# Kernel optimization log

Measured on AMD Instinct MI355X. Metric: run time of the kernel, lower is better.

Reference implementation:

```python
import jax, jax.numpy as jnp
import numpy as np

KS = 3  # kernel_size
N, C_IN, C_OUT, H, W = 8, 64, 128, 256, 256


def _grid_sample_bilinear(img, gx, gy):
    """img [C,H,W]; gx, gy [Ho,Wo] normalized coords; align_corners=False, zero padding."""
    C, H_, W_ = img.shape
    ix = ((gx + 1.0) * W_ - 1.0) / 2.0
    iy = ((gy + 1.0) * H_ - 1.0) / 2.0
    x0 = jnp.floor(ix); y0 = jnp.floor(iy)
    x1 = x0 + 1.0;      y1 = y0 + 1.0
    wx1 = ix - x0; wx0 = 1.0 - wx1
    wy1 = iy - y0; wy0 = 1.0 - wy1

    def gather(yi, xi):
        valid = (xi >= 0) & (xi < W_) & (yi >= 0) & (yi < H_)
        xc = jnp.clip(xi, 0, W_ - 1).astype(jnp.int32)
        yc = jnp.clip(yi, 0, H_ - 1).astype(jnp.int32)
        v = img[:, yc, xc]  # [C,Ho,Wo]
        return v * valid[None].astype(img.dtype)

    out = (gather(y0, x0) * (wy0 * wx0)[None]
         + gather(y0, x1) * (wy0 * wx1)[None]
         + gather(y1, x0) * (wy1 * wx0)[None]
         + gather(y1, x1) * (wy1 * wx1)[None])
    return out


def setup_inputs() -> dict:
    key = jax.random.key(0)
    k1, k2, k3 = jax.random.split(key, 3)
    x = jax.random.normal(k1, (N, C_IN, H, W), dtype=jnp.float32)
    # offset conv: Conv2d(inc, 2*ks, ks, padding=(ks-1)//2, bias=False)
    offset_w = jax.random.normal(k2, (2 * KS, C_IN, KS, KS), dtype=jnp.float32) * 0.05
    # conv_kernel: Conv2d(inc, outc, kernel=(ks,1), stride=(ks,1), bias=False), kaiming fan_out
    fan_out = C_OUT * KS * 1
    conv_w = jax.random.normal(k3, (C_OUT, C_IN, KS, 1), dtype=jnp.float32) * np.sqrt(2.0 / fan_out)
    return {"x": x, "offset_w": offset_w, "conv_w": conv_w}


def reference(x, offset_w, conv_w):
    n, c, h, w = x.shape
    ks = KS
    pad = (ks - 1) // 2
    dn = ('NCHW', 'OIHW', 'NCHW')

    off = jax.lax.conv_general_dilated(x, offset_w, (1, 1), ((pad, pad), (pad, pad)),
                                       dimension_numbers=dn)  # [n,2ks,h,w]
    off = jnp.tanh(off).reshape(n, 2, ks, h, w)
    offset_y = off[:, 0]  # [n,ks,h,w]; x offsets are computed but unused in the original

    yc = (ks - 1) // 2
    # cumulative offsets radiating outward from the center row
    upper = jnp.cumsum(offset_y[:, yc:], axis=1)                       # indices yc..ks-1
    lower = jnp.cumsum(offset_y[:, :yc + 1][:, ::-1], axis=1)[:, ::-1]  # indices 0..yc
    y_new = jnp.concatenate([lower[:, :yc], upper], axis=1)            # [n,ks,h,w]

    # base grid replicates torch's repeat-then-reshape layout exactly:
    # flat pattern [-1,0,1,-1,0,1,...] of length ks*h*w, reshaped to (ks,h,w)
    vals = jnp.arange(-(ks - 1) // 2, (ks - 1) // 2 + 1, dtype=x.dtype)
    base = vals[jnp.arange(ks * h * w) % ks].reshape(ks, h, w)

    grid_y = (base[None] + y_new).reshape(n, ks * h, w)
    gy = grid_y / ((h - 1.0) / 2.0) - 1.0
    gx = jnp.full_like(gy, -1.0)  # grid_x is zeros -> 0/((w-1)/2) - 1 = -1

    sampled = jax.vmap(_grid_sample_bilinear)(x, gx, gy)  # [n,c,ks*h,w]

    out = jax.lax.conv_general_dilated(sampled, conv_w, (ks, 1), ((0, 0), (0, 0)),
                                       dimension_numbers=dn)  # [n,outc,h,w]
    return out
```

## Files before the change

### kernel.cpp

```cpp
#include <hip/hip_runtime.h>
#include <math.h>

#define H 256
#define W 256
#define NB 8
#define CIN 64
#define COUT 128
#define G 2
#define CPG 32

typedef float f4v __attribute__((ext_vector_type(4)));

__global__ __launch_bounds__(256) void koffset(const float* __restrict__ x,
                                               const float* __restrict__ offw,
                                               float* __restrict__ part) {
    __shared__ float tile[2][34 * 40];
    const int g = blockIdx.z & (G - 1);
    const int n = blockIdx.z / G;
    const int i0 = blockIdx.y * 32;
    const int j0 = blockIdx.x * 32;
    const int tid = threadIdx.x;
    const int li = tid >> 3;
    const int lj4 = (tid & 7) * 4;

    const int a1 = tid / 10, cv1 = tid - a1 * 10;
    const int p2 = tid + 256;
    const int a2 = p2 / 10, cv2 = p2 - a2 * 10;
    const bool have2 = (p2 < 340);

    const float* xbase = x + ((size_t)(n * CIN + g * CPG)) * (H * W);

    auto ld = [&](int a, int cv, const float* xp) -> float4 {
        int gi = i0 - 1 + a;
        int gj = j0 - 4 + cv * 4;
        if ((unsigned)gi < (unsigned)H && (unsigned)gj < (unsigned)W)
            return *(const float4*)(xp + gi * W + gj);
        return make_float4(0.f, 0.f, 0.f, 0.f);
    };

    float acc[3][4];
#pragma unroll
    for (int k = 0; k < 3; ++k)
#pragma unroll
        for (int d = 0; d < 4; ++d) acc[k][d] = 0.f;

    float4 r1 = ld(a1, cv1, xbase);
    float4 r2 = have2 ? ld(a2, cv2, xbase) : make_float4(0, 0, 0, 0);

    for (int c = 0; c < CPG; ++c) {
        float* buf = tile[c & 1];
        *(float4*)(buf + tid * 4) = r1;
        if (have2) *(float4*)(buf + p2 * 4) = r2;
        float4 r1n, r2n;
        if (c < CPG - 1) {
            const float* xpn = xbase + (size_t)(c + 1) * (H * W);
            r1n = ld(a1, cv1, xpn);
            r2n = have2 ? ld(a2, cv2, xpn) : make_float4(0, 0, 0, 0);
        }
        __syncthreads();
        const float* wp = offw + (g * CPG + c) * 9;
#pragma unroll
        for (int u = 0; u < 3; ++u) {
            float row[6];
#pragma unroll
            for (int m = 0; m < 6; ++m) row[m] = buf[(li + u) * 40 + 3 + lj4 + m];
#pragma unroll
            for (int k = 0; k < 3; ++k) {
                float w0 = wp[k * 576 + u * 3 + 0];
                float w1 = wp[k * 576 + u * 3 + 1];
                float w2 = wp[k * 576 + u * 3 + 2];
#pragma unroll
                for (int d = 0; d < 4; ++d)
                    acc[k][d] += row[d] * w0 + row[d + 1] * w1 + row[d + 2] * w2;
            }
        }
        r1 = r1n;
        r2 = r2n;
    }

    size_t base = (((size_t)g * NB + n) * 3) * (H * W) + (size_t)(i0 + li) * W + (j0 + lj4);
#pragma unroll
    for (int k = 0; k < 3; ++k) {
        float4 o = make_float4(acc[k][0], acc[k][1], acc[k][2], acc[k][3]);
        *(float4*)(part + base + (size_t)k * (H * W)) = o;
    }
}

__global__ __launch_bounds__(256) void kreduce(const float* __restrict__ part,
                                               float* __restrict__ ynew) {
    int idx = blockIdx.x * 256 + threadIdx.x;
    int n = idx >> 14;
    int hw4 = idx & 16383;
    size_t off = (size_t)hw4 * 4;
    float t[3][4];
#pragma unroll
    for (int k = 0; k < 3; ++k) {
        float4 s0 = *(const float4*)(part + (((size_t)0 * NB + n) * 3 + k) * (H * W) + off);
        float4 s1 = *(const float4*)(part + (((size_t)1 * NB + n) * 3 + k) * (H * W) + off);
        t[k][0] = tanhf(s0.x + s1.x);
        t[k][1] = tanhf(s0.y + s1.y);
        t[k][2] = tanhf(s0.z + s1.z);
        t[k][3] = tanhf(s0.w + s1.w);
    }
    size_t base = ((size_t)n * 3) * (H * W) + off;
    *(float4*)(ynew + base) =
        make_float4(t[0][0] + t[1][0], t[0][1] + t[1][1], t[0][2] + t[1][2], t[0][3] + t[1][3]);
    *(float4*)(ynew + base + (size_t)(H * W)) = make_float4(t[1][0], t[1][1], t[1][2], t[1][3]);
    *(float4*)(ynew + base + (size_t)2 * (H * W)) =
        make_float4(t[1][0] + t[2][0], t[1][1] + t[2][1], t[1][2] + t[2][2], t[1][3] + t[2][3]);
}

__global__ __launch_bounds__(256) void kpmat(const float* __restrict__ x,
                                             const float* __restrict__ convw,
                                             float* __restrict__ P) {
    __shared__ float xl[CIN * 4];
    __shared__ float wl[16 * 192];
    const int n = blockIdx.x >> 3;
    const int co0 = (blockIdx.x & 7) * 16;
    const int tid = threadIdx.x;
    {
        int ci = tid >> 2, y = tid & 3;
        xl[tid] = x[(((size_t)n * CIN + ci) * H + y) * W];
    }
    for (int p = tid; p < 16 * 192; p += 256) wl[p] = convw[co0 * 192 + p];
    __syncthreads();
    if (tid < 192) {
        int co = tid / 12, t = tid - co * 12;
        int r = t >> 2, y = t & 3;
        float s = 0.f;
#pragma unroll
        for (int ci = 0; ci < CIN; ++ci) s += wl[co * 192 + ci * 3 + r] * xl[ci * 4 + y];
        P[((size_t)n * COUT + co0 + co) * 16 + t] = s;
    }
}

__global__ __launch_bounds__(256) void kout(const float* __restrict__ ynew,
                                            const float* __restrict__ P,
                                            float* __restrict__ out) {
    __shared__ float Cs[12 * 256];
    __shared__ float Pl[128 * 16];
    const int n = blockIdx.y;
    const int i = blockIdx.x;
    const int tid = threadIdx.x;

    {
        const f4v* src = (const f4v*)(P + (size_t)n * COUT * 16);
        f4v* dst = (f4v*)Pl;
        dst[tid] = src[tid];
        dst[tid + 256] = src[tid + 256];
    }

    {
        const int j = tid;
        float c[12];
#pragma unroll
        for (int t = 0; t < 12; ++t) c[t] = 0.f;
#pragma unroll
        for (int r = 0; r < 3; ++r) {
            int rowi = 3 * i + r;
            int k = rowi >> 8;
            int i2 = rowi & 255;
            float g = (float)(((k + i2 + j) % 3) - 1) +
                      ynew[((size_t)n * 3 + k) * (H * W) + i2 * W + j];
            float gy = g / 127.5f - 1.0f;
            float iy = ((gy + 1.0f) * 256.0f - 1.0f) * 0.5f;
            float fy = floorf(iy);
            int y0 = (int)fy;
            float w1 = iy - fy;
            if ((unsigned)y0 < 4u) c[r * 4 + y0] += 0.5f * (1.0f - w1);
            int y1 = y0 + 1;
            if ((unsigned)y1 < 4u) c[r * 4 + y1] += 0.5f * w1;
        }
#pragma unroll
        for (int t = 0; t < 12; ++t) Cs[t * 256 + j] = c[t];
    }
    __syncthreads();

    const int jq = (tid & 63) * 4;
    const int cg = tid >> 6;
    float4 cc[12];
#pragma unroll
    for (int t = 0; t < 12; ++t) cc[t] = *(const float4*)&Cs[t * 256 + jq];

    float* op = out + (((size_t)n * COUT) * H + i) * W;
    for (int co = cg * 32; co < cg * 32 + 32; ++co) {
        const float4* pp = (const float4*)&Pl[co * 16];
        float4 P0 = pp[0], P1 = pp[1], P2 = pp[2];
        float pv[12] = {P0.x, P0.y, P0.z, P0.w, P1.x, P1.y, P1.z, P1.w,
                        P2.x, P2.y, P2.z, P2.w};
        f4v a = {0.f, 0.f, 0.f, 0.f};
#pragma unroll
        for (int t = 0; t < 12; ++t) {
            a.x += pv[t] * cc[t].x;
            a.y += pv[t] * cc[t].y;
            a.z += pv[t] * cc[t].z;
            a.w += pv[t] * cc[t].w;
        }
        __builtin_nontemporal_store(a, (f4v*)(op + (size_t)co * (H * W) + jq));
    }
}

extern "C" void kernel_launch(void* const* d_in, const int* in_sizes, int n_in,
                              void* d_out, int out_size, void* d_ws, size_t ws_size,
                              hipStream_t stream) {
    const float* x = (const float*)d_in[0];
    const float* offw = (const float*)d_in[1];
    const float* convw = (const float*)d_in[2];
    float* out = (float*)d_out;

    const size_t PART_FLOATS = (size_t)G * NB * 3 * H * W;
    const size_t YNEW_FLOATS = (size_t)NB * 3 * H * W;
    float* part = (float*)d_ws;
    float* ynew = part + PART_FLOATS;
    float* P = ynew + YNEW_FLOATS;

    koffset<<<dim3(8, 8, NB * G), 256, 0, stream>>>(x, offw, part);
    kreduce<<<dim3(NB * H * W / 4 / 256), 256, 0, stream>>>(part, ynew);
    kpmat<<<dim3(64), 256, 0, stream>>>(x, convw, P);
    kout<<<dim3(H, NB), 256, 0, stream>>>(ynew, P, out);
}
```

Measured before the change: 392.8 us.

## Fuse offset conv with tanh/cumsum reduction using per-wave tiles over all channels

Drops the two-group channel split and the separate reduction kernel. The offset convolution now covers all 64 input channels in one block and applies tanh and the cumulative offsets directly, so the partial-sum buffer never goes through global memory. Each wavefront owns an 8-row slice with its own double-buffered LDS tile and no block-wide barrier, and it reads LDS rows as float4. The cost is half as many blocks (512 instead of 1024) and a longer serial channel loop per block, which lowers parallelism.

```diff
diff --git a/kernel.cpp b/kernel.cpp
--- a/kernel.cpp
+++ b/kernel.cpp
@@ -6,37 +6,45 @@
 #define NB 8
 #define CIN 64
 #define COUT 128
-#define G 2
-#define CPG 32
+#define HW (H * W)
 
 typedef float f4v __attribute__((ext_vector_type(4)));
 
-__global__ __launch_bounds__(256) void koffset(const float* __restrict__ x,
-                                               const float* __restrict__ offw,
-                                               float* __restrict__ part) {
-    __shared__ float tile[2][34 * 40];
-    const int g = blockIdx.z & (G - 1);
-    const int n = blockIdx.z / G;
+__global__ __launch_bounds__(256) void koffset2(const float* __restrict__ x,
+                                                const float* __restrict__ offw,
+                                                float* __restrict__ ynew) {
+    __shared__ float tile[4][2][10 * 40];
+    const int n = blockIdx.z;
     const int i0 = blockIdx.y * 32;
     const int j0 = blockIdx.x * 32;
     const int tid = threadIdx.x;
-    const int li = tid >> 3;
-    const int lj4 = (tid & 7) * 4;
-
-    const int a1 = tid / 10, cv1 = tid - a1 * 10;
-    const int p2 = tid + 256;
-    const int a2 = p2 / 10, cv2 = p2 - a2 * 10;
-    const bool have2 = (p2 < 340);
-
-    const float* xbase = x + ((size_t)(n * CIN + g * CPG)) * (H * W);
-
-    auto ld = [&](int a, int cv, const float* xp) -> float4 {
-        int gi = i0 - 1 + a;
-        int gj = j0 - 4 + cv * 4;
-        if ((unsigned)gi < (unsigned)H && (unsigned)gj < (unsigned)W)
-            return *(const float4*)(xp + gi * W + gj);
-        return make_float4(0.f, 0.f, 0.f, 0.f);
-    };
+    const int wv = tid >> 6;
+    const int lane = tid & 63;
+    const int rloc = lane >> 3;
+    const int lj4 = (lane & 7) << 2;
+    const int iw0 = i0 + 8 * wv - 1;
+
+    const int a1 = lane / 10, q1 = lane - a1 * 10;
+    const int gi1 = iw0 + a1, gj1 = j0 - 4 + 4 * q1;
+    const bool v1 = ((unsigned)gi1 < (unsigned)H) && ((unsigned)gj1 < (unsigned)W);
+    const size_t off1 = v1 ? ((size_t)gi1 * W + gj1) : 0;
+
+    const int s2 = lane + 64;
+    const int a2 = s2 / 10, q2 = s2 - a2 * 10;
+    const int gi2 = iw0 + a2, gj2 = j0 - 4 + 4 * q2;
+    const bool hv2 = (s2 < 100);
+    const bool v2 = hv2 && ((unsigned)gi2 < (unsigned)H) && ((unsigned)gj2 < (unsigned)W);
+    const size_t off2 = v2 ? ((size_t)gi2 * W + gj2) : 0;
+
+    const float* xn = x + (size_t)n * CIN * HW;
+    const float4 zf4 = make_float4(0.f, 0.f, 0.f, 0.f);
+
+    float4 ra1 = v1 ? *(const float4*)(xn + off1) : zf4;
+    float4 ra2 = v2 ? *(const float4*)(xn + off2) : zf4;
+    float4 rb1 = v1 ? *(const float4*)(xn + HW + off1) : zf4;
+    float4 rb2 = v2 ? *(const float4*)(xn + HW + off2) : zf4;
+    const float* p1 = xn + 2 * HW + off1;
+    const float* p2 = xn + 2 * HW + off2;
 
     float acc[3][4];
 #pragma unroll
@@ -44,70 +52,60 @@
 #pragma unroll
         for (int d = 0; d < 4; ++d) acc[k][d] = 0.f;
 
-    float4 r1 = ld(a1, cv1, xbase);
-    float4 r2 = have2 ? ld(a2, cv2, xbase) : make_float4(0, 0, 0, 0);
-
-    for (int c = 0; c < CPG; ++c) {
-        float* buf = tile[c & 1];
-        *(float4*)(buf + tid * 4) = r1;
-        if (have2) *(float4*)(buf + p2 * 4) = r2;
-        float4 r1n, r2n;
-        if (c < CPG - 1) {
-            const float* xpn = xbase + (size_t)(c + 1) * (H * W);
-            r1n = ld(a1, cv1, xpn);
-            r2n = have2 ? ld(a2, cv2, xpn) : make_float4(0, 0, 0, 0);
-        }
-        __syncthreads();
-        const float* wp = offw + (g * CPG + c) * 9;
-#pragma unroll
-        for (int u = 0; u < 3; ++u) {
-            float row[6];
-#pragma unroll
-            for (int m = 0; m < 6; ++m) row[m] = buf[(li + u) * 40 + 3 + lj4 + m];
-#pragma unroll
-            for (int k = 0; k < 3; ++k) {
-                float w0 = wp[k * 576 + u * 3 + 0];
-                float w1 = wp[k * 576 + u * 3 + 1];
-                float w2 = wp[k * 576 + u * 3 + 2];
-#pragma unroll
-                for (int d = 0; d < 4; ++d)
-                    acc[k][d] += row[d] * w0 + row[d + 1] * w1 + row[d + 2] * w2;
+    float* buf0 = &tile[wv][0][0];
+    float* buf1 = &tile[wv][1][0];
+
+    for (int c = 0; c < CIN; c += 2) {
+#pragma unroll
+        for (int h = 0; h < 2; ++h) {
+            float* buf = h ? buf1 : buf0;
+            *(float4*)(buf + 4 * lane) = ra1;
+            if (hv2) *(float4*)(buf + 4 * s2) = ra2;
+            ra1 = rb1;
+            ra2 = rb2;
+            if (c + h + 2 < CIN) {
+                rb1 = v1 ? *(const float4*)p1 : zf4;
+                rb2 = v2 ? *(const float4*)p2 : zf4;
+                p1 += HW;
+                p2 += HW;
+            }
+            const float* wp = offw + (size_t)(c + h) * 9;
+#pragma unroll
+            for (int u = 0; u < 3; ++u) {
+                const float* rp = buf + (rloc + u) * 40 + lj4;
+                float4 b0 = *(const float4*)(rp);
+                float4 b1 = *(const float4*)(rp + 4);
+                float4 b2 = *(const float4*)(rp + 8);
+                const float r0 = b0.w, r1 = b1.x, r2 = b1.y, r3 = b1.z, r4 = b1.w, r5 = b2.x;
+#pragma unroll
+                for (int k = 0; k < 3; ++k) {
+                    const float w0 = wp[k * 576 + u * 3 + 0];
+                    const float w1 = wp[k * 576 + u * 3 + 1];
+                    const float w2 = wp[k * 576 + u * 3 + 2];
+                    acc[k][0] += r0 * w0 + r1 * w1 + r2 * w2;
+                    acc[k][1] += r1 * w0 + r2 * w1 + r3 * w2;
+                    acc[k][2] += r2 * w0 + r3 * w1 + r4 * w2;
+                    acc[k][3] += r3 * w0 + r4 * w1 + r5 * w2;
+                }
             }
         }
-        r1 = r1n;
-        r2 = r2n;
-    }
-
-    size_t base = (((size_t)g * NB + n) * 3) * (H * W) + (size_t)(i0 + li) * W + (j0 + lj4);
-#pragma unroll
-    for (int k = 0; k < 3; ++k) {
-        float4 o = make_float4(acc[k][0], acc[k][1], acc[k][2], acc[k][3]);
-        *(float4*)(part + base + (size_t)k * (H * W)) = o;
-    }
-}
-
-__global__ __launch_bounds__(256) void kreduce(const float* __restrict__ part,
-                                               float* __restrict__ ynew) {
-    int idx = blockIdx.x * 256 + threadIdx.x;
-    int n = idx >> 14;
-    int hw4 = idx & 16383;
-    size_t off = (size_t)hw4 * 4;
-    float t[3][4];
-#pragma unroll
-    for (int k = 0; k < 3; ++k) {
-        float4 s0 = *(const float4*)(part + (((size_t)0 * NB + n) * 3 + k) * (H * W) + off);
-        float4 s1 = *(const float4*)(part + (((size_t)1 * NB + n) * 3 + k) * (H * W) + off);
-        t[k][0] = tanhf(s0.x + s1.x);
-        t[k][1] = tanhf(s0.y + s1.y);
-        t[k][2] = tanhf(s0.z + s1.z);
-        t[k][3] = tanhf(s0.w + s1.w);
-    }
-    size_t base = ((size_t)n * 3) * (H * W) + off;
-    *(float4*)(ynew + base) =
-        make_float4(t[0][0] + t[1][0], t[0][1] + t[1][1], t[0][2] + t[1][2], t[0][3] + t[1][3]);
-    *(float4*)(ynew + base + (size_t)(H * W)) = make_float4(t[1][0], t[1][1], t[1][2], t[1][3]);
-    *(float4*)(ynew + base + (size_t)2 * (H * W)) =
-        make_float4(t[1][0] + t[2][0], t[1][1] + t[2][1], t[1][2] + t[2][2], t[1][3] + t[2][3]);
+    }
+
+    float y[3][4];
+#pragma unroll
+    for (int d = 0; d < 4; ++d) {
+        float t0 = tanhf(acc[0][d]);
+        float t1 = tanhf(acc[1][d]);
+        float t2 = tanhf(acc[2][d]);
+        y[0][d] = t0 + t1;
+        y[1][d] = t1;
+        y[2][d] = t1 + t2;
+    }
+    size_t base = (size_t)n * 3 * HW + (size_t)(i0 + 8 * wv + rloc) * W + (j0 + lj4);
+#pragma unroll
+    for (int k = 0; k < 3; ++k)
+        *(float4*)(ynew + base + (size_t)k * HW) =
+            make_float4(y[k][0], y[k][1], y[k][2], y[k][3]);
 }
 
 __global__ __launch_bounds__(256) void kpmat(const float* __restrict__ x,
@@ -208,14 +206,10 @@
     const float* convw = (const float*)d_in[2];
     float* out = (float*)d_out;
 
-    const size_t PART_FLOATS = (size_t)G * NB * 3 * H * W;
-    const size_t YNEW_FLOATS = (size_t)NB * 3 * H * W;
-    float* part = (float*)d_ws;
-    float* ynew = part + PART_FLOATS;
-    float* P = ynew + YNEW_FLOATS;
-
-    koffset<<<dim3(8, 8, NB * G), 256, 0, stream>>>(x, offw, part);
-    kreduce<<<dim3(NB * H * W / 4 / 256), 256, 0, stream>>>(part, ynew);
+    float* ynew = (float*)d_ws;
+    float* P = ynew + (size_t)NB * 3 * HW;
+
+    koffset2<<<dim3(8, 8, NB), 256, 0, stream>>>(x, offw, ynew);
     kpmat<<<dim3(64), 256, 0, stream>>>(x, convw, P);
     kout<<<dim3(H, NB), 256, 0, stream>>>(ynew, P, out);
 }
```

Result: no change. 391.2 us (-0.4%).
